# Performance work log

Hardware: AMD Instinct MI355X
Metric: run time of the kernel (lower is better)

The kernel has to match this reference:

```python
import jax, jax.numpy as jnp
import numpy as np

N = 4_000_000

def quat_to_rotmat(q):
    # q: (N,4) normalized [w,x,y,z] -> (N,3,3)
    w, x, y, z = q[:, 0], q[:, 1], q[:, 2], q[:, 3]
    R = jnp.stack([
        jnp.stack([1 - 2*y*y - 2*z*z, 2*x*y - 2*w*z,     2*x*z + 2*w*y],     axis=1),
        jnp.stack([2*x*y + 2*w*z,     1 - 2*x*x - 2*z*z, 2*y*z - 2*w*x],     axis=1),
        jnp.stack([2*x*z - 2*w*y,     2*y*z + 2*w*x,     1 - 2*x*x - 2*y*y], axis=1),
    ], axis=1)
    return R

def setup_inputs() -> dict:
    key = jax.random.key(0)
    k1, k2 = jax.random.split(key)
    rotation_raw = jax.random.normal(k1, (N, 4), dtype=jnp.float32)
    scaling_raw = jax.random.normal(k2, (N, 3), dtype=jnp.float32)
    return {"rotation_raw": rotation_raw, "scaling_raw": scaling_raw}

def reference(rotation_raw, scaling_raw):
    # F.normalize(quat, dim=-1)
    q = rotation_raw / jnp.linalg.norm(rotation_raw, axis=-1, keepdims=True)
    R = quat_to_rotmat(q)                      # (N,3,3)
    s = jnp.exp(scaling_raw)                   # (N,3) scaling = exp activation
    RS = R * s[:, None, :]                     # R @ diag(s): scale columns
    cov = jnp.einsum('nik,njk->nij', RS, RS)   # RS @ RS^T
    return cov
```

## Files before the change

### kernel.cpp

```cpp
#include <hip/hip_runtime.h>
#include <hip/hip_bf16.h>


static __device__ __forceinline__ void cov_point(
    float w, float x, float y, float z,
    float s0, float s1, float s2, float c[9])
{
    float inv = rsqrtf(w * w + x * x + y * y + z * z);
    w *= inv; x *= inv; y *= inv; z *= inv;

    float r00 = 1.f - 2.f * (y * y + z * z);
    float r01 = 2.f * (x * y - w * z);
    float r02 = 2.f * (x * z + w * y);
    float r10 = 2.f * (x * y + w * z);
    float r11 = 1.f - 2.f * (x * x + z * z);
    float r12 = 2.f * (y * z - w * x);
    float r20 = 2.f * (x * z - w * y);
    float r21 = 2.f * (y * z + w * x);
    float r22 = 1.f - 2.f * (x * x + y * y);

    float t0 = __expf(2.f * s0);
    float t1 = __expf(2.f * s1);
    float t2 = __expf(2.f * s2);

    c[0] = r00 * r00 * t0 + r01 * r01 * t1 + r02 * r02 * t2;
    c[1] = r00 * r10 * t0 + r01 * r11 * t1 + r02 * r12 * t2;
    c[2] = r00 * r20 * t0 + r01 * r21 * t1 + r02 * r22 * t2;
    c[3] = c[1];
    c[4] = r10 * r10 * t0 + r11 * r11 * t1 + r12 * r12 * t2;
    c[5] = r10 * r20 * t0 + r11 * r21 * t1 + r12 * r22 * t2;
    c[6] = c[2];
    c[7] = c[5];
    c[8] = r20 * r20 * t0 + r21 * r21 * t1 + r22 * r22 * t2;
}

__global__ __launch_bounds__(256) void gaussian_cov_kernel(
    const float4* __restrict__ rot,
    const float2* __restrict__ sca,
    float2* __restrict__ out,
    int npairs)
{
    int t = blockIdx.x * blockDim.x + threadIdx.x;
    if (t >= npairs) return;

    float4 q0 = rot[2 * t + 0];
    float4 q1 = rot[2 * t + 1];
    float2 f0 = sca[3 * t + 0];
    float2 f1 = sca[3 * t + 1];
    float2 f2 = sca[3 * t + 2];

    float c0[9], c1[9];
    cov_point(q0.x, q0.y, q0.z, q0.w, f0.x, f0.y, f1.x, c0);
    cov_point(q1.x, q1.y, q1.z, q1.w, f1.y, f2.x, f2.y, c1);

    float2* o = out + (size_t)9 * (size_t)t;
    o[0] = make_float2(c0[0], c0[1]);
    o[1] = make_float2(c0[2], c0[3]);
    o[2] = make_float2(c0[4], c0[5]);
    o[3] = make_float2(c0[6], c0[7]);
    o[4] = make_float2(c0[8], c1[0]);
    o[5] = make_float2(c1[1], c1[2]);
    o[6] = make_float2(c1[3], c1[4]);
    o[7] = make_float2(c1[5], c1[6]);
    o[8] = make_float2(c1[7], c1[8]);
}

__global__ void gaussian_cov_tail(
    const float* __restrict__ rot,
    const float* __restrict__ sca,
    float* __restrict__ out,
    int idx)
{
    float c[9];
    cov_point(rot[4 * idx + 0], rot[4 * idx + 1], rot[4 * idx + 2], rot[4 * idx + 3],
              sca[3 * idx + 0], sca[3 * idx + 1], sca[3 * idx + 2], c);
    for (int k = 0; k < 9; ++k)
        out[9 * idx + k] = c[k];
}

extern "C" void kernel_launch(void* const* d_in, const int* in_sizes, int n_in,
                              void* d_out, int out_size, void* d_ws, size_t ws_size,
                              hipStream_t stream) {
    const int n = in_sizes[0] / 4;
    const int npairs = n / 2;

    const float4* rot = (const float4*)d_in[0];
    const float2* sca = (const float2*)d_in[1];
    float2* out = (float2*)d_out;

    const int block = 256;
    const int grid = (npairs + block - 1) / block;
    gaussian_cov_kernel<<<grid, block, 0, stream>>>(rot, sca, out, npairs);

    if (n & 1) {
        gaussian_cov_tail<<<1, 1, 0, stream>>>(
            (const float*)d_in[0], (const float*)d_in[1],
            (float*)d_out, n - 1);
    }
}
```

Before: 249.5 us.

## Stage inputs and outputs through LDS for fully coalesced float4 global access

Each block now stages 512 points' quaternions and scales into shared memory with float4 loads, computes covariances from LDS, writes results back to LDS, then streams the block's outputs to global memory as contiguous float4 stores. The goal is to replace the strided float2 per-thread accesses with coalesced wide transactions on this bandwidth-bound kernel, and it also drops the separate tail kernel launch. In exchange it adds three barriers and 18KB of LDS per block, which may limit occupancy. The strided per-thread LDS reads and writes (stride 6 and 18 floats) may also cause bank conflicts.

```diff
diff --git a/kernel.cpp b/kernel.cpp
--- a/kernel.cpp
+++ b/kernel.cpp
@@ -1,6 +1,9 @@
 #include <hip/hip_runtime.h>
 #include <hip/hip_bf16.h>
 
+
+#define TPB 256
+#define PPB 512
 
 static __device__ __forceinline__ void cov_point(
     float w, float x, float y, float z,
@@ -34,67 +37,87 @@
     c[8] = r20 * r20 * t0 + r21 * r21 * t1 + r22 * r22 * t2;
 }
 
-__global__ __launch_bounds__(256) void gaussian_cov_kernel(
-    const float4* __restrict__ rot,
-    const float2* __restrict__ sca,
-    float2* __restrict__ out,
-    int npairs)
+__global__ __launch_bounds__(TPB) void gaussian_cov_kernel(
+    const float4* __restrict__ rot4,
+    const float4* __restrict__ sca4,
+    const float*  __restrict__ sca_f,
+    float4* __restrict__ out4,
+    float*  __restrict__ out_f,
+    int n)
 {
-    int t = blockIdx.x * blockDim.x + threadIdx.x;
-    if (t >= npairs) return;
+    __shared__ float lds[PPB * 9];
 
-    float4 q0 = rot[2 * t + 0];
-    float4 q1 = rot[2 * t + 1];
-    float2 f0 = sca[3 * t + 0];
-    float2 f1 = sca[3 * t + 1];
-    float2 f2 = sca[3 * t + 2];
+    const int tid  = threadIdx.x;
+    const int base = blockIdx.x * PPB;
+    const int n_pt = min(PPB, n - base);
+
+    float4* lrot  = (float4*)lds;
+    float*  lsca  = lds + 4 * PPB;
+    float4* lsca4 = (float4*)lsca;
+
+    for (int idx = tid; idx < n_pt; idx += TPB)
+        lrot[idx] = rot4[base + idx];
+
+    const int nsf = 3 * n_pt;
+    const int ns4 = nsf >> 2;
+    const float4* gsca4 = sca4 + ((3 * base) >> 2);
+    for (int idx = tid; idx < ns4; idx += TPB)
+        lsca4[idx] = gsca4[idx];
+    if (tid < (nsf & 3))
+        lsca[(ns4 << 2) + tid] = sca_f[3 * base + (ns4 << 2) + tid];
+
+    __syncthreads();
+
+    const int j0 = 2 * tid;
+    const bool act0 = (j0 < n_pt);
+    const bool act1 = (j0 + 1 < n_pt);
 
     float c0[9], c1[9];
-    cov_point(q0.x, q0.y, q0.z, q0.w, f0.x, f0.y, f1.x, c0);
-    cov_point(q1.x, q1.y, q1.z, q1.w, f1.y, f2.x, f2.y, c1);
+    if (act0) {
+        float4 q = lrot[j0];
+        float s0 = lsca[6 * tid + 0], s1 = lsca[6 * tid + 1], s2 = lsca[6 * tid + 2];
+        cov_point(q.x, q.y, q.z, q.w, s0, s1, s2, c0);
+    }
+    if (act1) {
+        float4 q = lrot[j0 + 1];
+        float s3 = lsca[6 * tid + 3], s4 = lsca[6 * tid + 4], s5 = lsca[6 * tid + 5];
+        cov_point(q.x, q.y, q.z, q.w, s3, s4, s5, c1);
+    }
 
-    float2* o = out + (size_t)9 * (size_t)t;
-    o[0] = make_float2(c0[0], c0[1]);
-    o[1] = make_float2(c0[2], c0[3]);
-    o[2] = make_float2(c0[4], c0[5]);
-    o[3] = make_float2(c0[6], c0[7]);
-    o[4] = make_float2(c0[8], c1[0]);
-    o[5] = make_float2(c1[1], c1[2]);
-    o[6] = make_float2(c1[3], c1[4]);
-    o[7] = make_float2(c1[5], c1[6]);
-    o[8] = make_float2(c1[7], c1[8]);
-}
+    __syncthreads();
 
-__global__ void gaussian_cov_tail(
-    const float* __restrict__ rot,
-    const float* __restrict__ sca,
-    float* __restrict__ out,
-    int idx)
-{
-    float c[9];
-    cov_point(rot[4 * idx + 0], rot[4 * idx + 1], rot[4 * idx + 2], rot[4 * idx + 3],
-              sca[3 * idx + 0], sca[3 * idx + 1], sca[3 * idx + 2], c);
-    for (int k = 0; k < 9; ++k)
-        out[9 * idx + k] = c[k];
+    if (act0) {
+        #pragma unroll
+        for (int m = 0; m < 9; ++m) lds[18 * tid + m] = c0[m];
+    }
+    if (act1) {
+        #pragma unroll
+        for (int m = 0; m < 9; ++m) lds[18 * tid + 9 + m] = c1[m];
+    }
+
+    __syncthreads();
+
+    const int nof = 9 * n_pt;
+    const int no4 = nof >> 2;
+    float4* lout4 = (float4*)lds;
+    float4* gout4 = out4 + ((9 * (size_t)base) >> 2);
+    for (int idx = tid; idx < no4; idx += TPB)
+        gout4[idx] = lout4[idx];
+    if (tid < (nof & 3))
+        out_f[9 * (size_t)base + (no4 << 2) + tid] = lds[(no4 << 2) + tid];
 }
 
 extern "C" void kernel_launch(void* const* d_in, const int* in_sizes, int n_in,
                               void* d_out, int out_size, void* d_ws, size_t ws_size,
                               hipStream_t stream) {
     const int n = in_sizes[0] / 4;
-    const int npairs = n / 2;
 
-    const float4* rot = (const float4*)d_in[0];
-    const float2* sca = (const float2*)d_in[1];
-    float2* out = (float2*)d_out;
+    const float4* rot4 = (const float4*)d_in[0];
+    const float4* sca4 = (const float4*)d_in[1];
+    const float*  scaf = (const float*)d_in[1];
+    float4* out4 = (float4*)d_out;
+    float*  outf = (float*)d_out;
 
-    const int block = 256;
-    const int grid = (npairs + block - 1) / block;
-    gaussian_cov_kernel<<<grid, block, 0, stream>>>(rot, sca, out, npairs);
-
-    if (n & 1) {
-        gaussian_cov_tail<<<1, 1, 0, stream>>>(
-            (const float*)d_in[0], (const float*)d_in[1],
-            (float*)d_out, n - 1);
-    }
+    const int grid = (n + PPB - 1) / PPB;
+    gaussian_cov_kernel<<<grid, TPB, 0, stream>>>(rot4, sca4, scaf, out4, outf, n);
 }
```

Result: faster. 229.5 us (-8.0%).
